# Performance work log

Measured on AMD Instinct MI355X. Metric: run time of the kernel, lower is better.

## Reference

```python
import jax, jax.numpy as jnp
import numpy as np

B, S, H, NH = 2, 2048, 2048, 16
HD = H // NH
SCALE = 1.0 / np.sqrt(HD).astype(np.float32)


def setup_inputs() -> dict:
    key = jax.random.key(0)
    ks = jax.random.split(key, 11)
    std = 1.0 / np.sqrt(H)
    inp = {
        'query': jax.random.normal(ks[0], (B, S, H), dtype=jnp.float32),
        'key': jax.random.normal(ks[1], (B, S, H), dtype=jnp.float32),
        'value': jax.random.normal(ks[2], (B, S, H), dtype=jnp.float32),
        'Wq': jax.random.normal(ks[3], (H, H), dtype=jnp.float32) * std,
        'bq': jax.random.normal(ks[4], (H,), dtype=jnp.float32) * std,
        'Wk': jax.random.normal(ks[5], (H, H), dtype=jnp.float32) * std,
        'bk': jax.random.normal(ks[6], (H,), dtype=jnp.float32) * std,
        'Wv': jax.random.normal(ks[7], (H, H), dtype=jnp.float32) * std,
        'bv': jax.random.normal(ks[8], (H,), dtype=jnp.float32) * std,
        'Wo': jax.random.normal(ks[9], (H, H), dtype=jnp.float32) * std,
        'bo': jax.random.normal(ks[10], (H,), dtype=jnp.float32) * std,
    }
    return inp


def reference(query, key, value, Wq, bq, Wk, bk, Wv, bv, Wo, bo):
    # Linear projections (torch Linear: x @ W.T + b)
    q = query @ Wq.T + bq
    k = key @ Wk.T + bk
    v = value @ Wv.T + bv
    # [B, NH, S, HD]
    q = q.reshape(B, S, NH, HD).transpose(0, 2, 1, 3)
    k = k.reshape(B, S, NH, HD).transpose(0, 2, 1, 3)
    v = v.reshape(B, S, NH, HD).transpose(0, 2, 1, 3)
    scores = jnp.einsum('bhqd,bhkd->bhqk', q, k) * SCALE
    attn = jax.nn.softmax(scores, axis=-1)  # dropout p=0 (eval)
    ctx = jnp.einsum('bhqk,bhkd->bhqd', attn, v)
    ctx = ctx.transpose(0, 2, 1, 3).reshape(B, S, H)
    out = ctx @ Wo.T + bo
    return out
```

## Files before the change

### kernel.cpp

```cpp
#include <hip/hip_runtime.h>


typedef __bf16 bf16_t;
typedef __bf16 bf16x8 __attribute__((ext_vector_type(8)));
typedef float  f32x4  __attribute__((ext_vector_type(4)));

#define DEVI __device__ __forceinline__

DEVI void async_copy16(const void* gsrc, void* ldst) {
  __builtin_amdgcn_global_load_lds(
      (const __attribute__((address_space(1))) unsigned int*)gsrc,
      (__attribute__((address_space(3))) unsigned int*)ldst, 16, 0, 0);
}

constexpr int Bc = 2, Sc = 2048, Hc = 2048, NHc = 16, HDc = 128;
constexpr float SCALE_LOG2E = 0.12751744550358464f;
constexpr int PSTR = 72;

DEVI void cast_body(const float* __restrict__ in, bf16_t* __restrict__ out) {
  int i = (blockIdx.x * 256 + threadIdx.x) * 8;
  float4 f0 = *(const float4*)(in + i);
  float4 f1 = *(const float4*)(in + i + 4);
  union { bf16_t h[8]; uint4 u; } o;
  o.h[0] = (bf16_t)f0.x; o.h[1] = (bf16_t)f0.y;
  o.h[2] = (bf16_t)f0.z; o.h[3] = (bf16_t)f0.w;
  o.h[4] = (bf16_t)f1.x; o.h[5] = (bf16_t)f1.y;
  o.h[6] = (bf16_t)f1.z; o.h[7] = (bf16_t)f1.w;
  *(uint4*)(out + i) = o.u;
}

__global__ void cast3(const float* __restrict__ a, const float* __restrict__ b,
                      const float* __restrict__ c, bf16_t* __restrict__ oa,
                      bf16_t* __restrict__ ob, bf16_t* __restrict__ oc) {
  const float* src = blockIdx.y == 0 ? a : blockIdx.y == 1 ? b : c;
  bf16_t* dst = blockIdx.y == 0 ? oa : blockIdx.y == 1 ? ob : oc;
  cast_body(src, dst);
}

__global__ void cast4(const float* __restrict__ a, const float* __restrict__ b,
                      const float* __restrict__ c, const float* __restrict__ d,
                      bf16_t* __restrict__ oa, bf16_t* __restrict__ ob,
                      bf16_t* __restrict__ oc, bf16_t* __restrict__ od) {
  const float* src = blockIdx.y == 0 ? a : blockIdx.y == 1 ? b
                   : blockIdx.y == 2 ? c : d;
  bf16_t* dst = blockIdx.y == 0 ? oa : blockIdx.y == 1 ? ob
              : blockIdx.y == 2 ? oc : od;
  cast_body(src, dst);
}

template <int M, int N, int K>
DEVI void gemm_body(const bf16_t* __restrict__ A, const bf16_t* __restrict__ Bw,
                    const float* __restrict__ bias, void* __restrict__ Cout,
                    float scale, int out_mode) {
  constexpr int BM = 256, BN = 128, BK = 64;
  constexpr int NT = K / BK;
  constexpr int SLOT = (BM + BN) * BK;
  __shared__ __align__(16) bf16_t lds[3 * SLOT];

  const int tid = threadIdx.x;
  const int lane = tid & 63;
  const int wave = tid >> 6;
  const int bm = blockIdx.x & (M / BM - 1);
  const int bn = blockIdx.x / (M / BM);
  const int wm = wave >> 1, wn = wave & 1;
  const int quad = lane >> 4, l15 = lane & 15;

  const bf16_t* Abase = A + (size_t)bm * BM * K;
  const bf16_t* Bbase = Bw + (size_t)bn * BN * K;
  const bf16_t* asrc0; const bf16_t* asrc1; const bf16_t* asrc2; const bf16_t* asrc3;
  const bf16_t* bsrc0; const bf16_t* bsrc1;
  int aoff0, aoff1, aoff2, aoff3, boff0, boff1;
  {
    int i0 = wave * 4;
    int r0 = i0 * 8 + (lane >> 3);       aoff0 = i0 * 512;
    int r1 = (i0 + 1) * 8 + (lane >> 3); aoff1 = (i0 + 1) * 512;
    int r2 = (i0 + 2) * 8 + (lane >> 3); aoff2 = (i0 + 2) * 512;
    int r3 = (i0 + 3) * 8 + (lane >> 3); aoff3 = (i0 + 3) * 512;
    asrc0 = Abase + (size_t)r0 * K + (((lane & 7) ^ (r0 & 7)) * 8);
    asrc1 = Abase + (size_t)r1 * K + (((lane & 7) ^ (r1 & 7)) * 8);
    asrc2 = Abase + (size_t)r2 * K + (((lane & 7) ^ (r2 & 7)) * 8);
    asrc3 = Abase + (size_t)r3 * K + (((lane & 7) ^ (r3 & 7)) * 8);
    int j0 = wave * 2;
    int s0 = j0 * 8 + (lane >> 3);       boff0 = BM * BK + j0 * 512;
    int s1 = (j0 + 1) * 8 + (lane >> 3); boff1 = BM * BK + (j0 + 1) * 512;
    bsrc0 = Bbase + (size_t)s0 * K + (((lane & 7) ^ (s0 & 7)) * 8);
    bsrc1 = Bbase + (size_t)s1 * K + (((lane & 7) ^ (s1 & 7)) * 8);
  }

  f32x4 zero4 = {0.f, 0.f, 0.f, 0.f};
  f32x4 acc[4][4];
#pragma unroll
  for (int i = 0; i < 4; ++i)
#pragma unroll
    for (int j = 0; j < 4; ++j) acc[i][j] = zero4;

  int arow[4], brow[4];
#pragma unroll
  for (int t = 0; t < 4; ++t) {
    arow[t] = wm * 64 + t * 16 + l15;
    brow[t] = wn * 64 + t * 16 + l15;
  }

  auto stage_half0 = [&](int kt) {
    bf16_t* slot = lds + (kt % 3) * SLOT;
    int k0 = kt * BK;
    async_copy16(asrc0 + k0, slot + aoff0);
    async_copy16(asrc1 + k0, slot + aoff1);
    async_copy16(bsrc0 + k0, slot + boff0);
  };
  auto stage_half1 = [&](int kt) {
    bf16_t* slot = lds + (kt % 3) * SLOT;
    int k0 = kt * BK;
    async_copy16(asrc2 + k0, slot + aoff2);
    async_copy16(asrc3 + k0, slot + aoff3);
    async_copy16(bsrc1 + k0, slot + boff1);
  };

  stage_half0(0); stage_half1(0);
  stage_half0(1); stage_half1(1);

  for (int kt = 0; kt < NT; ++kt) {
    if (kt + 1 < NT) {
      asm volatile("s_waitcnt vmcnt(6)" ::: "memory");
    } else {
      asm volatile("s_waitcnt vmcnt(0)" ::: "memory");
    }
    __builtin_amdgcn_s_barrier();
    asm volatile("" ::: "memory");

    const bf16_t* As = lds + (kt % 3) * SLOT;
    const bf16_t* Bs = As + BM * BK;
    const bool do_stage = (kt + 2 < NT);

#pragma unroll
    for (int ks = 0; ks < 2; ++ks) {
      if (do_stage) {
        if (ks == 0) stage_half0(kt + 2);
        else         stage_half1(kt + 2);
      }
      bf16x8 af[4], bfv[4];
#pragma unroll
      for (int mt = 0; mt < 4; ++mt)
        af[mt] = *(const bf16x8*)(As + arow[mt] * 64 +
                                  (((ks * 4 + quad) ^ (arow[mt] & 7)) * 8));
#pragma unroll
      for (int nt = 0; nt < 4; ++nt)
        bfv[nt] = *(const bf16x8*)(Bs + brow[nt] * 64 +
                                   (((ks * 4 + quad) ^ (brow[nt] & 7)) * 8));
      __builtin_amdgcn_s_setprio(1);
#pragma unroll
      for (int mt = 0; mt < 4; ++mt)
#pragma unroll
        for (int nt = 0; nt < 4; ++nt)
          acc[mt][nt] = __builtin_amdgcn_mfma_f32_16x16x32_bf16(
              af[mt], bfv[nt], acc[mt][nt], 0, 0, 0);
      __builtin_amdgcn_s_setprio(0);
    }
  }

  float bv[4];
#pragma unroll
  for (int nt = 0; nt < 4; ++nt) bv[nt] = bias[bn * BN + brow[nt]];

#pragma unroll
  for (int mt = 0; mt < 4; ++mt) {
    const int rbase = bm * BM + wm * 64 + mt * 16 + quad * 4;
#pragma unroll
    for (int nt = 0; nt < 4; ++nt) {
      const int col = bn * BN + brow[nt];
      if (out_mode == 0) {
        bf16_t* C = (bf16_t*)Cout;
#pragma unroll
        for (int r = 0; r < 4; ++r)
          C[(size_t)(rbase + r) * N + col] = (bf16_t)((acc[mt][nt][r] + bv[nt]) * scale);
      } else if (out_mode == 2) {
        float* C = (float*)Cout;
#pragma unroll
        for (int r = 0; r < 4; ++r)
          C[(size_t)(rbase + r) * N + col] = acc[mt][nt][r] + bv[nt];
      } else {
        bf16_t* C = (bf16_t*)Cout;
        const int bb = rbase >> 11;
        const int s0 = rbase & (Sc - 1);
        const int h = col >> 7, d = col & (HDc - 1);
        union { bf16_t h4[4]; uint2 u; } o;
#pragma unroll
        for (int r = 0; r < 4; ++r) o.h4[r] = (bf16_t)(acc[mt][nt][r] + bv[nt]);
        *(uint2*)(C + (((size_t)(bb * NHc + h) * HDc + d) * Sc + s0)) = o.u;
      }
    }
  }
}

__global__ __launch_bounds__(512, 2) void qkv_proj(
    const bf16_t* __restrict__ Xq, const bf16_t* __restrict__ Xk,
    const bf16_t* __restrict__ Xv, const bf16_t* __restrict__ Wq,
    const bf16_t* __restrict__ Wk, const bf16_t* __restrict__ Wv,
    const float* __restrict__ bq, const float* __restrict__ bk,
    const float* __restrict__ bv, bf16_t* __restrict__ q,
    bf16_t* __restrict__ k, bf16_t* __restrict__ vt) {
  const int p = blockIdx.y;
  const bf16_t* A = p == 0 ? Xq : p == 1 ? Xk : Xv;
  const bf16_t* W = p == 0 ? Wq : p == 1 ? Wk : Wv;
  const float* bi = p == 0 ? bq : p == 1 ? bk : bv;
  void* out = p == 0 ? (void*)q : p == 1 ? (void*)k : (void*)vt;
  gemm_body<4096, 2048, 2048>(A, W, bi, out, p == 0 ? SCALE_LOG2E : 1.0f,
                              p == 2 ? 1 : 0);
}

__global__ __launch_bounds__(512, 2) void o_proj(
    const bf16_t* __restrict__ A, const bf16_t* __restrict__ W,
    const float* __restrict__ bi, float* __restrict__ out) {
  gemm_body<4096, 2048, 2048>(A, W, bi, out, 1.0f, 2);
}

__global__ __launch_bounds__(256, 2) void flash_attn(const bf16_t* __restrict__ Q,
                                                     const bf16_t* __restrict__ Kg,
                                                     const bf16_t* __restrict__ Vt,
                                                     bf16_t* __restrict__ ctx) {
  __shared__ __align__(16) bf16_t smem[2 * 64 * 128 + 128 * 64 + 4 * 32 * PSTR];
  bf16_t* Ks0 = smem;
  bf16_t* Ks1 = smem + 8192;
  bf16_t* Vs = smem + 16384;
  bf16_t* Ps = smem + 24576;

  const int tid = threadIdx.x, lane = tid & 63, wave = tid >> 6;
  const int quad = lane >> 4, l15 = lane & 15;
  const int bid = blockIdx.x;
  const int qt = bid & 15, h = (bid >> 4) & 15, b = bid >> 8;

  bf16_t* Pw = Ps + wave * (32 * PSTR);

  bf16x8 qf[2][4];
#pragma unroll
  for (int mt = 0; mt < 2; ++mt) {
    int grow = b * Sc + qt * 128 + wave * 32 + mt * 16 + l15;
    const bf16_t* qp = Q + (size_t)grow * Hc + h * HDc;
#pragma unroll
    for (int kc = 0; kc < 4; ++kc) qf[mt][kc] = *(const bf16x8*)(qp + kc * 32 + quad * 8);
  }

  f32x4 zero4 = {0.f, 0.f, 0.f, 0.f};
  f32x4 o[2][8];
#pragma unroll
  for (int mt = 0; mt < 2; ++mt)
#pragma unroll
    for (int dt = 0; dt < 8; ++dt) o[mt][dt] = zero4;
  float mrow[2][4], lpart[2][4];
#pragma unroll
  for (int mt = 0; mt < 2; ++mt)
#pragma unroll
    for (int r = 0; r < 4; ++r) { mrow[mt][r] = -1e30f; lpart[mt][r] = 0.f; }

  int kr_[4], kc_[4], vr_[4], vc_[4];
#pragma unroll
  for (int i = 0; i < 4; ++i) {
    int s = wave * 4 + i;
    kr_[i] = s * 4 + quad;        kc_[i] = l15 ^ (kr_[i] & 7);
    vr_[i] = s * 8 + (lane >> 3); vc_[i] = (lane & 7) ^ (vr_[i] & 7);
  }
  const bf16_t* Kbase = Kg + (size_t)b * Sc * Hc + h * HDc;
  const bf16_t* Vbase = Vt + (size_t)(b * NHc + h) * HDc * Sc;

  auto stageK = [&](int kb, bf16_t* dst) {
#pragma unroll
    for (int i = 0; i < 4; ++i)
      async_copy16(Kbase + (size_t)(kb * 64 + kr_[i]) * Hc + kc_[i] * 8,
                   dst + (wave * 4 + i) * 512);
  };
  auto stageV = [&](int kb) {
#pragma unroll
    for (int i = 0; i < 4; ++i)
      async_copy16(Vbase + (size_t)vr_[i] * Sc + kb * 64 + vc_[i] * 8,
                   Vs + (wave * 4 + i) * 512);
  };

  stageK(0, Ks0);
  stageV(0);
  stageK(1, Ks1);

  for (int kb = 0; kb < 32; ++kb) {
    bf16_t* Kcur = (kb & 1) ? Ks1 : Ks0;

    if (kb + 1 < 32) asm volatile("s_waitcnt vmcnt(8)" ::: "memory");
    else             asm volatile("s_waitcnt vmcnt(4)" ::: "memory");
    __builtin_amdgcn_s_barrier();
    asm volatile("" ::: "memory");

    f32x4 sf[2][4];
#pragma unroll
    for (int mt = 0; mt < 2; ++mt)
#pragma unroll
      for (int nt = 0; nt < 4; ++nt) sf[mt][nt] = zero4;
#pragma unroll
    for (int kc = 0; kc < 4; ++kc)
#pragma unroll
      for (int nt = 0; nt < 4; ++nt) {
        int kr = nt * 16 + l15;
        bf16x8 kf = *(const bf16x8*)(Kcur + kr * 128 + (((kc * 4 + quad) ^ (kr & 7)) * 8));
        sf[0][nt] = __builtin_amdgcn_mfma_f32_16x16x32_bf16(qf[0][kc], kf, sf[0][nt], 0, 0, 0);
        sf[1][nt] = __builtin_amdgcn_mfma_f32_16x16x32_bf16(qf[1][kc], kf, sf[1][nt], 0, 0, 0);
      }

    float mx[2][4];
    bool need = false;
#pragma unroll
    for (int mt = 0; mt < 2; ++mt)
#pragma unroll
      for (int r = 0; r < 4; ++r) {
        float m0 = fmaxf(fmaxf(sf[mt][0][r], sf[mt][1][r]),
                         fmaxf(sf[mt][2][r], sf[mt][3][r]));
#pragma unroll
        for (int off = 1; off < 16; off <<= 1) m0 = fmaxf(m0, __shfl_xor(m0, off));
        mx[mt][r] = m0;
        need = need || (m0 > mrow[mt][r] + 8.0f);
      }
    if (__any(need)) {
#pragma unroll
      for (int mt = 0; mt < 2; ++mt)
#pragma unroll
        for (int r = 0; r < 4; ++r) {
          float mnew = fmaxf(mrow[mt][r], mx[mt][r]);
          float alpha = __builtin_amdgcn_exp2f(mrow[mt][r] - mnew);
          mrow[mt][r] = mnew;
          lpart[mt][r] *= alpha;
#pragma unroll
          for (int dt = 0; dt < 8; ++dt) o[mt][dt][r] *= alpha;
        }
    }
#pragma unroll
    for (int mt = 0; mt < 2; ++mt)
#pragma unroll
      for (int r = 0; r < 4; ++r) {
        float p0 = __builtin_amdgcn_exp2f(sf[mt][0][r] - mrow[mt][r]);
        float p1 = __builtin_amdgcn_exp2f(sf[mt][1][r] - mrow[mt][r]);
        float p2 = __builtin_amdgcn_exp2f(sf[mt][2][r] - mrow[mt][r]);
        float p3 = __builtin_amdgcn_exp2f(sf[mt][3][r] - mrow[mt][r]);
        sf[mt][0][r] = p0; sf[mt][1][r] = p1;
        sf[mt][2][r] = p2; sf[mt][3][r] = p3;
        lpart[mt][r] += (p0 + p1) + (p2 + p3);
      }

#pragma unroll
    for (int mt = 0; mt < 2; ++mt)
#pragma unroll
      for (int nt = 0; nt < 4; ++nt)
#pragma unroll
        for (int r = 0; r < 4; ++r)
          Pw[(mt * 16 + quad * 4 + r) * PSTR + nt * 16 + l15] = (bf16_t)sf[mt][nt][r];

    bf16x8 pf[2][2];
#pragma unroll
    for (int mt = 0; mt < 2; ++mt) {
      const bf16_t* pr = Pw + (mt * 16 + l15) * PSTR;
#pragma unroll
      for (int kc = 0; kc < 2; ++kc)
        pf[mt][kc] = *(const bf16x8*)(pr + kc * 32 + quad * 8);
    }

    if (kb + 1 < 32) asm volatile("s_waitcnt vmcnt(4)" ::: "memory");
    else             asm volatile("s_waitcnt vmcnt(0)" ::: "memory");
    __builtin_amdgcn_s_barrier();
    asm volatile("" ::: "memory");

#pragma unroll
    for (int kc = 0; kc < 2; ++kc)
#pragma unroll
      for (int dt = 0; dt < 8; ++dt) {
        int vr = dt * 16 + l15;
        bf16x8 vf = *(const bf16x8*)(Vs + vr * 64 + (((kc * 4 + quad) ^ (vr & 7)) * 8));
        o[0][dt] = __builtin_amdgcn_mfma_f32_16x16x32_bf16(pf[0][kc], vf, o[0][dt], 0, 0, 0);
        o[1][dt] = __builtin_amdgcn_mfma_f32_16x16x32_bf16(pf[1][kc], vf, o[1][dt], 0, 0, 0);
      }

    __builtin_amdgcn_s_barrier();
    asm volatile("" ::: "memory");
    if (kb + 1 < 32) stageV(kb + 1);
    if (kb + 2 < 32) stageK(kb + 2, Kcur);
  }

  __syncthreads();
  bf16_t* Ow = smem + wave * 4096;
#pragma unroll
  for (int mt = 0; mt < 2; ++mt) {
    float rinv[4];
#pragma unroll
    for (int r = 0; r < 4; ++r) {
      float l = lpart[mt][r];
#pragma unroll
      for (int off = 1; off < 16; off <<= 1) l += __shfl_xor(l, off);
      rinv[r] = 1.f / l;
    }
#pragma unroll
    for (int dt = 0; dt < 8; ++dt)
#pragma unroll
      for (int r = 0; r < 4; ++r)
        Ow[(mt * 16 + quad * 4 + r) * 128 + dt * 16 + l15] = (bf16_t)(o[mt][dt][r] * rinv[r]);
  }
#pragma unroll
  for (int r = 0; r < 32; ++r) {
    unsigned v = *(const unsigned*)(Ow + r * 128 + lane * 2);
    int grow = b * Sc + qt * 128 + wave * 32 + r;
    *(unsigned*)(ctx + (size_t)grow * Hc + h * HDc + lane * 2) = v;
  }
}

extern "C" void kernel_launch(void* const* d_in, const int* in_sizes, int n_in,
                              void* d_out, int out_size, void* d_ws, size_t ws_size,
                              hipStream_t stream) {
  const float* query = (const float*)d_in[0];
  const float* key_i = (const float*)d_in[1];
  const float* value = (const float*)d_in[2];
  const float* Wq = (const float*)d_in[3];
  const float* bq = (const float*)d_in[4];
  const float* Wk = (const float*)d_in[5];
  const float* bk = (const float*)d_in[6];
  const float* Wv = (const float*)d_in[7];
  const float* bv = (const float*)d_in[8];
  const float* Wo = (const float*)d_in[9];
  const float* bo = (const float*)d_in[10];

  const size_t XE = (size_t)Bc * Sc * Hc;
  const size_t WE = (size_t)Hc * Hc;
  const size_t need = 6 * XE * 2 + 4 * WE * 2;
  if (ws_size < need) return;

  char* ws = (char*)d_ws;
  size_t off = 0;
  auto alloc = [&](size_t bytes) {
    char* p = ws + off;
    off += (bytes + 255) & ~(size_t)255;
    return p;
  };
  bf16_t* Xq = (bf16_t*)alloc(XE * 2);
  bf16_t* Xk = (bf16_t*)alloc(XE * 2);
  bf16_t* Xv = (bf16_t*)alloc(XE * 2);
  bf16_t* Wqb = (bf16_t*)alloc(WE * 2);
  bf16_t* Wkb = (bf16_t*)alloc(WE * 2);
  bf16_t* Wvb = (bf16_t*)alloc(WE * 2);
  bf16_t* Wob = (bf16_t*)alloc(WE * 2);
  bf16_t* qb = (bf16_t*)alloc(XE * 2);
  bf16_t* kb = (bf16_t*)alloc(XE * 2);
  bf16_t* vtb = (bf16_t*)alloc(XE * 2);
  bf16_t* ctxb = Xq;

  cast3<<<dim3((unsigned)(XE / 2048), 3), 256, 0, stream>>>(query, key_i, value, Xq, Xk, Xv);
  cast4<<<dim3((unsigned)(WE / 2048), 4), 256, 0, stream>>>(Wq, Wk, Wv, Wo, Wqb, Wkb, Wvb, Wob);

  qkv_proj<<<dim3(256, 3), 512, 0, stream>>>(Xq, Xk, Xv, Wqb, Wkb, Wvb,
                                             bq, bk, bv, qb, kb, vtb);

  flash_attn<<<512, 256, 0, stream>>>(qb, kb, vtb, ctxb);

  o_proj<<<256, 512, 0, stream>>>(ctxb, Wob, bo, (float*)d_out);
}
```

Baseline: 462.8 us.

## Restructure GEMM wave layout into 2x4 with ping-pong fragment loads and block remap

The GEMM body now arranges its eight waves as 2x4 instead of 4x2, so each wave computes a 128x32 sub-tile. Each k-tile is processed in two halves: fragments are loaded, the next async stage is issued, and a barrier is followed by a batch of MFMAs under raised priority, with sched_barrier fences keeping the ordering. Block indices are also remapped with a stride-8 interleave to change L2 reuse across blocks. The intent is to overlap LDS reads, global loads and MFMA work between waves, at the cost of extra barriers per iteration and a block mapping that assumes a 256-block grid.

```diff
diff --git a/kernel.cpp b/kernel.cpp
--- a/kernel.cpp
+++ b/kernel.cpp
@@ -60,9 +60,10 @@
   const int tid = threadIdx.x;
   const int lane = tid & 63;
   const int wave = tid >> 6;
-  const int bm = blockIdx.x & (M / BM - 1);
-  const int bn = blockIdx.x / (M / BM);
-  const int wm = wave >> 1, wn = wave & 1;
+  const int lid = (blockIdx.x & 7) * 32 + (blockIdx.x >> 3);
+  const int bm = lid & (M / BM - 1);
+  const int bn = lid / (M / BM);
+  const int wm = wave >> 2, wn = wave & 3;
   const int quad = lane >> 4, l15 = lane & 15;
 
   const bf16_t* Abase = A + (size_t)bm * BM * K;
@@ -88,18 +89,11 @@
   }
 
   f32x4 zero4 = {0.f, 0.f, 0.f, 0.f};
-  f32x4 acc[4][4];
-#pragma unroll
-  for (int i = 0; i < 4; ++i)
-#pragma unroll
-    for (int j = 0; j < 4; ++j) acc[i][j] = zero4;
-
-  int arow[4], brow[4];
-#pragma unroll
-  for (int t = 0; t < 4; ++t) {
-    arow[t] = wm * 64 + t * 16 + l15;
-    brow[t] = wn * 64 + t * 16 + l15;
-  }
+  f32x4 acc[8][2];
+#pragma unroll
+  for (int i = 0; i < 8; ++i)
+#pragma unroll
+    for (int j = 0; j < 2; ++j) acc[i][j] = zero4;
 
   auto stage_half0 = [&](int kt) {
     bf16_t* slot = lds + (kt % 3) * SLOT;
@@ -132,52 +126,82 @@
     const bf16_t* Bs = As + BM * BK;
     const bool do_stage = (kt + 2 < NT);
 
-#pragma unroll
-    for (int ks = 0; ks < 2; ++ks) {
-      if (do_stage) {
-        if (ks == 0) stage_half0(kt + 2);
-        else         stage_half1(kt + 2);
-      }
-      bf16x8 af[4], bfv[4];
-#pragma unroll
-      for (int mt = 0; mt < 4; ++mt)
-        af[mt] = *(const bf16x8*)(As + arow[mt] * 64 +
-                                  (((ks * 4 + quad) ^ (arow[mt] & 7)) * 8));
-#pragma unroll
-      for (int nt = 0; nt < 4; ++nt)
-        bfv[nt] = *(const bf16x8*)(Bs + brow[nt] * 64 +
-                                   (((ks * 4 + quad) ^ (brow[nt] & 7)) * 8));
-      __builtin_amdgcn_s_setprio(1);
-#pragma unroll
-      for (int mt = 0; mt < 4; ++mt)
-#pragma unroll
-        for (int nt = 0; nt < 4; ++nt)
-          acc[mt][nt] = __builtin_amdgcn_mfma_f32_16x16x32_bf16(
-              af[mt], bfv[nt], acc[mt][nt], 0, 0, 0);
-      __builtin_amdgcn_s_setprio(0);
-    }
-  }
-
-  float bv[4];
-#pragma unroll
-  for (int nt = 0; nt < 4; ++nt) bv[nt] = bias[bn * BN + brow[nt]];
-
-#pragma unroll
-  for (int mt = 0; mt < 4; ++mt) {
-    const int rbase = bm * BM + wm * 64 + mt * 16 + quad * 4;
-#pragma unroll
-    for (int nt = 0; nt < 4; ++nt) {
-      const int col = bn * BN + brow[nt];
+    bf16x8 afr[4][2], bfr[2][2];
+
+#pragma unroll
+    for (int m = 0; m < 4; ++m) {
+      int ar = wm * 128 + m * 16 + l15;
+#pragma unroll
+      for (int ks = 0; ks < 2; ++ks)
+        afr[m][ks] = *(const bf16x8*)(As + ar * 64 + (((ks * 4 + quad) ^ (ar & 7)) * 8));
+    }
+#pragma unroll
+    for (int n = 0; n < 2; ++n) {
+      int br = wn * 32 + n * 16 + l15;
+#pragma unroll
+      for (int ks = 0; ks < 2; ++ks)
+        bfr[n][ks] = *(const bf16x8*)(Bs + br * 64 + (((ks * 4 + quad) ^ (br & 7)) * 8));
+    }
+    if (do_stage) stage_half0(kt + 2);
+    __builtin_amdgcn_s_barrier();
+    asm volatile("s_waitcnt lgkmcnt(0)" ::: "memory");
+    __builtin_amdgcn_sched_barrier(0);
+    __builtin_amdgcn_s_setprio(1);
+#pragma unroll
+    for (int m = 0; m < 4; ++m)
+#pragma unroll
+      for (int n = 0; n < 2; ++n)
+#pragma unroll
+        for (int ks = 0; ks < 2; ++ks)
+          acc[m][n] = __builtin_amdgcn_mfma_f32_16x16x32_bf16(
+              afr[m][ks], bfr[n][ks], acc[m][n], 0, 0, 0);
+    __builtin_amdgcn_s_setprio(0);
+    __builtin_amdgcn_s_barrier();
+    asm volatile("" ::: "memory");
+
+#pragma unroll
+    for (int m = 0; m < 4; ++m) {
+      int ar = wm * 128 + (m + 4) * 16 + l15;
+#pragma unroll
+      for (int ks = 0; ks < 2; ++ks)
+        afr[m][ks] = *(const bf16x8*)(As + ar * 64 + (((ks * 4 + quad) ^ (ar & 7)) * 8));
+    }
+    if (do_stage) stage_half1(kt + 2);
+    __builtin_amdgcn_s_barrier();
+    asm volatile("s_waitcnt lgkmcnt(0)" ::: "memory");
+    __builtin_amdgcn_sched_barrier(0);
+    __builtin_amdgcn_s_setprio(1);
+#pragma unroll
+    for (int m = 0; m < 4; ++m)
+#pragma unroll
+      for (int n = 0; n < 2; ++n)
+#pragma unroll
+        for (int ks = 0; ks < 2; ++ks)
+          acc[m + 4][n] = __builtin_amdgcn_mfma_f32_16x16x32_bf16(
+              afr[m][ks], bfr[n][ks], acc[m + 4][n], 0, 0, 0);
+    __builtin_amdgcn_s_setprio(0);
+  }
+
+  float bv2[2];
+#pragma unroll
+  for (int n = 0; n < 2; ++n) bv2[n] = bias[bn * BN + wn * 32 + n * 16 + l15];
+
+#pragma unroll
+  for (int m = 0; m < 8; ++m) {
+    const int rbase = bm * BM + wm * 128 + m * 16 + quad * 4;
+#pragma unroll
+    for (int n = 0; n < 2; ++n) {
+      const int col = bn * BN + wn * 32 + n * 16 + l15;
       if (out_mode == 0) {
         bf16_t* C = (bf16_t*)Cout;
 #pragma unroll
         for (int r = 0; r < 4; ++r)
-          C[(size_t)(rbase + r) * N + col] = (bf16_t)((acc[mt][nt][r] + bv[nt]) * scale);
+          C[(size_t)(rbase + r) * N + col] = (bf16_t)((acc[m][n][r] + bv2[n]) * scale);
       } else if (out_mode == 2) {
         float* C = (float*)Cout;
 #pragma unroll
         for (int r = 0; r < 4; ++r)
-          C[(size_t)(rbase + r) * N + col] = acc[mt][nt][r] + bv[nt];
+          C[(size_t)(rbase + r) * N + col] = acc[m][n][r] + bv2[n];
       } else {
         bf16_t* C = (bf16_t*)Cout;
         const int bb = rbase >> 11;
@@ -185,7 +209,7 @@
         const int h = col >> 7, d = col & (HDc - 1);
         union { bf16_t h4[4]; uint2 u; } o;
 #pragma unroll
-        for (int r = 0; r < 4; ++r) o.h4[r] = (bf16_t)(acc[mt][nt][r] + bv[nt]);
+        for (int r = 0; r < 4; ++r) o.h4[r] = (bf16_t)(acc[m][n][r] + bv2[n]);
         *(uint2*)(C + (((size_t)(bb * NHc + h) * HDc + d) * Sc + s0)) = o.u;
       }
     }
```

New measurement: 464.1 us. About the same (+0.3%).
